# Kernel optimization log

Hardware: AMD Instinct MI355X
Metric: run time of the kernel (lower is better)

The kernel has to match this reference:

```python
import jax, jax.numpy as jnp
import numpy as np

BS, N, C = 16, 4096, 32
HID, OUT = 16, 1
N_ORBS = 64


def _linear_init(key, fan_in, fan_out):
    # torch nn.Linear default: U(-1/sqrt(fan_in), 1/sqrt(fan_in)) for W and b
    kw, kb = jax.random.split(key)
    bound = 1.0 / np.sqrt(fan_in)
    W = jax.random.uniform(kw, (fan_in, fan_out), minval=-bound, maxval=bound, dtype=jnp.float32)
    b = jax.random.uniform(kb, (fan_out,), minval=-bound, maxval=bound, dtype=jnp.float32)
    return W, b


def setup_inputs() -> dict:
    key = jax.random.key(0)
    ks = jax.random.split(key, 8)
    coords = jax.random.normal(ks[0], (BS, N, 2, 2), dtype=jnp.float32)
    # orbit identifiers live at coords[:, :, 1, 1]; draw from a fixed discrete set
    orb_ids = jax.random.randint(ks[1], (BS, N), 0, N_ORBS).astype(jnp.float32)
    # guarantee all N_ORBS values appear so unique() has exactly N_ORBS entries
    orb_ids = orb_ids.at[0, :N_ORBS].set(jnp.arange(N_ORBS, dtype=jnp.float32))
    coords = coords.at[:, :, 1, 1].set(orb_ids)
    vals = jax.random.normal(ks[2], (BS, N, C), dtype=jnp.float32)
    mask = jax.random.bernoulli(ks[3], 0.9, (BS, N))
    W1, b1 = _linear_init(ks[4], C, HID)
    W2, b2 = _linear_init(ks[5], HID, HID)
    W3, b3 = _linear_init(ks[6], HID, OUT)
    return {"coords": coords, "vals": vals, "mask": mask,
            "W1": W1, "b1": b1, "W2": W2, "b2": b2, "W3": W3, "b3": b3,
            "n_orbs": N_ORBS}


def reference(coords, vals, mask, W1, b1, W2, b2, W3, b3, n_orbs):
    orb = coords[:, :, 1, 1]                              # (bs, n)
    # torch.unique over the whole tensor -> sorted global unique orbit values
    uniq = jnp.unique(orb, size=n_orbs)                   # (n_orbs,)
    # orbit-membership mask; einsum contraction over n == masked broadcast + sum(dim=1)
    orbs_mask = (orb[:, :, None] == uniq[None, None, :]).astype(vals.dtype)  # (bs, n, n_orbs)
    masked_vals = jnp.where(mask[..., None], vals, jnp.zeros((), vals.dtype))  # (bs, n, c)
    agg_orbs = jnp.einsum('bnk,bnc->bkc', orbs_mask, masked_vals)              # (bs, n_orbs, c)
    empty_orbs = agg_orbs.sum(axis=-1) == 0               # (bs, n_orbs)
    h = jax.nn.relu(agg_orbs @ W1 + b1)
    h = jax.nn.relu(h @ W2 + b2)
    transf = h @ W3 + b3                                  # (bs, n_orbs, out_dim)
    transf = jnp.where(empty_orbs[..., None], jnp.zeros((), transf.dtype), transf)
    return transf.sum(axis=1)                             # (bs, out_dim)
```

## Files before the change

### kernel.cpp

```cpp
#include <hip/hip_runtime.h>

#define BS     16
#define NPTS   4096
#define CH     32
#define HID    16
#define NORB   64
#define SLICES 16
#define PPB    (NPTS / SLICES)

__global__ __launch_bounds__(256) void gigp_agg(
    const float* __restrict__ coords,
    const float* __restrict__ vals,
    const int*   __restrict__ mask,
    float*       __restrict__ part)
{
    __shared__ float vlds[PPB][CH];
    __shared__ int   klds[PPB];

    const int tid   = threadIdx.x;
    const int b     = blockIdx.x >> 4;
    const int slice = blockIdx.x & (SLICES - 1);
    const size_t gbase = (size_t)b * NPTS + slice * PPB;

    const float4* v4  = (const float4*)vals + gbase * (CH / 4);
    float4*       vl4 = (float4*)&vlds[0][0];
    #pragma unroll
    for (int i = 0; i < PPB * CH / (4 * 256); ++i)
        vl4[tid + i * 256] = v4[tid + i * 256];

    {
        const size_t gi = gbase + tid;
        const int k = (int)coords[gi * 4 + 3];
        klds[tid] = mask[gi] ? k : NORB;
    }
    __syncthreads();

    const int myk  = tid >> 2;
    const int c0   = (tid & 3) * 8;
    const int lane = tid & 63;
    const int wo_s = __builtin_amdgcn_readfirstlane((tid >> 6) << 4);

    float acc[8] = {0, 0, 0, 0, 0, 0, 0, 0};

    for (int base = 0; base < PPB; base += 64) {
        const int kreg = klds[base + lane];
        #pragma unroll 8
        for (int j = 0; j < 64; ++j) {
            const int kn = __builtin_amdgcn_readlane(kreg, j);
            if ((unsigned)(kn - wo_s) < 16u) {
                if (kn == myk) {
                    const float4 u0 = *(const float4*)&vlds[base + j][c0];
                    const float4 u1 = *(const float4*)&vlds[base + j][c0 + 4];
                    acc[0] += u0.x; acc[1] += u0.y; acc[2] += u0.z; acc[3] += u0.w;
                    acc[4] += u1.x; acc[5] += u1.y; acc[6] += u1.z; acc[7] += u1.w;
                }
            }
        }
    }

    float4* dst = (float4*)(part + ((size_t)b * SLICES + slice) * NORB * CH);
    const int fi = myk * 8 + (tid & 3) * 2;
    dst[fi]     = make_float4(acc[0], acc[1], acc[2], acc[3]);
    dst[fi + 1] = make_float4(acc[4], acc[5], acc[6], acc[7]);
}

__global__ __launch_bounds__(256) void gigp_mlp(
    const float* __restrict__ part,
    const float* __restrict__ W1, const float* __restrict__ b1,
    const float* __restrict__ W2, const float* __restrict__ b2,
    const float* __restrict__ W3, const float* __restrict__ b3,
    float*       __restrict__ out)
{
    __shared__ float agg[NORB][CH + 1];
    __shared__ float wbuf[832];
    const int b   = blockIdx.x;
    const int tid = threadIdx.x;

    for (int i = tid; i < 817; i += 256) {
        float w;
        if      (i < 512) w = W1[i];
        else if (i < 528) w = b1[i - 512];
        else if (i < 784) w = W2[i - 528];
        else if (i < 800) w = b2[i - 784];
        else if (i < 816) w = W3[i - 800];
        else              w = b3[0];
        wbuf[i] = w;
    }

    const float4* src = (const float4*)(part + (size_t)b * SLICES * NORB * CH);
    float4 a0 = make_float4(0.f, 0.f, 0.f, 0.f);
    float4 a1 = make_float4(0.f, 0.f, 0.f, 0.f);
    #pragma unroll
    for (int s = 0; s < SLICES; ++s) {
        const float4 t0 = src[s * (NORB * CH / 4) + tid];
        const float4 t1 = src[s * (NORB * CH / 4) + tid + 256];
        a0.x += t0.x; a0.y += t0.y; a0.z += t0.z; a0.w += t0.w;
        a1.x += t1.x; a1.y += t1.y; a1.z += t1.z; a1.w += t1.w;
    }
    {
        const int e0 = tid, e1 = tid + 256;
        const int k0 = e0 >> 3, c0 = (e0 & 7) * 4;
        const int k1 = e1 >> 3, c1 = (e1 & 7) * 4;
        agg[k0][c0 + 0] = a0.x; agg[k0][c0 + 1] = a0.y;
        agg[k0][c0 + 2] = a0.z; agg[k0][c0 + 3] = a0.w;
        agg[k1][c1 + 0] = a1.x; agg[k1][c1 + 1] = a1.y;
        agg[k1][c1 + 2] = a1.z; agg[k1][c1 + 3] = a1.w;
    }
    __syncthreads();

    if (tid < NORB) {
        const int k = tid;
        const float* Wl1 = wbuf;
        const float* bl1 = wbuf + 512;
        const float* Wl2 = wbuf + 528;
        const float* bl2 = wbuf + 784;
        const float* Wl3 = wbuf + 800;
        const float  bl3 = wbuf[816];

        float chsum = 0.0f;
        #pragma unroll
        for (int cc = 0; cc < CH; ++cc) chsum += agg[k][cc];

        float h1[HID];
        #pragma unroll
        for (int j = 0; j < HID; ++j) h1[j] = bl1[j];
        #pragma unroll
        for (int cc = 0; cc < CH; ++cc) {
            const float x = agg[k][cc];
            #pragma unroll
            for (int j = 0; j < HID; ++j)
                h1[j] += x * Wl1[cc * HID + j];
        }
        #pragma unroll
        for (int j = 0; j < HID; ++j) h1[j] = h1[j] > 0.0f ? h1[j] : 0.0f;

        float h2[HID];
        #pragma unroll
        for (int j = 0; j < HID; ++j) h2[j] = bl2[j];
        #pragma unroll
        for (int i = 0; i < HID; ++i) {
            const float x = h1[i];
            #pragma unroll
            for (int j = 0; j < HID; ++j)
                h2[j] += x * Wl2[i * HID + j];
        }
        float o = bl3;
        #pragma unroll
        for (int i = 0; i < HID; ++i) {
            const float x = h2[i] > 0.0f ? h2[i] : 0.0f;
            o += x * Wl3[i];
        }
        o = (chsum == 0.0f) ? 0.0f : o;

        #pragma unroll
        for (int off = 32; off > 0; off >>= 1)
            o += __shfl_down(o, off);
        if (k == 0) out[b] = o;
    }
}

extern "C" void kernel_launch(void* const* d_in, const int* in_sizes, int n_in,
                              void* d_out, int out_size, void* d_ws, size_t ws_size,
                              hipStream_t stream) {
    const float* coords = (const float*)d_in[0];
    const float* vals   = (const float*)d_in[1];
    const int*   mask   = (const int*)d_in[2];
    const float* W1     = (const float*)d_in[3];
    const float* b1     = (const float*)d_in[4];
    const float* W2     = (const float*)d_in[5];
    const float* b2     = (const float*)d_in[6];
    const float* W3     = (const float*)d_in[7];
    const float* b3     = (const float*)d_in[8];
    float* out  = (float*)d_out;
    float* part = (float*)d_ws;

    gigp_agg<<<BS * SLICES, 256, 0, stream>>>(coords, vals, mask, part);
    gigp_mlp<<<BS, 256, 0, stream>>>(part, W1, b1, W2, b2, W3, b3, out);
}
```

Before: 98.05 us.

## Fuse aggregation and MLP kernels via cooperative grid sync

Merges the two kernels into one cooperative launch. Every block writes its partial sums, the whole grid synchronizes, and then the first BS blocks reduce the partials and run the MLP. This removes a kernel launch and the gap between the two dependent kernels. In exchange it adds a grid-wide barrier, uses more LDS per block, and depends on all 256 blocks being co-resident.

```diff
diff --git a/kernel.cpp b/kernel.cpp
--- a/kernel.cpp
+++ b/kernel.cpp
@@ -1,4 +1,7 @@
 #include <hip/hip_runtime.h>
+#include <hip/hip_cooperative_groups.h>
+
+namespace cg = cooperative_groups;
 
 #define BS     16
 #define NPTS   4096
@@ -8,18 +11,24 @@
 #define SLICES 16
 #define PPB    (NPTS / SLICES)
 
-__global__ __launch_bounds__(256) void gigp_agg(
+__global__ __launch_bounds__(256) void gigp_fused(
     const float* __restrict__ coords,
     const float* __restrict__ vals,
     const int*   __restrict__ mask,
-    float*       __restrict__ part)
+    float*       __restrict__ part,
+    const float* __restrict__ W1, const float* __restrict__ b1,
+    const float* __restrict__ W2, const float* __restrict__ b2,
+    const float* __restrict__ W3, const float* __restrict__ b3,
+    float*       __restrict__ out)
 {
     __shared__ float vlds[PPB][CH];
     __shared__ int   klds[PPB];
-
+    __shared__ float agg[NORB][CH + 1];
+    __shared__ float wbuf[832];
     const int tid   = threadIdx.x;
-    const int b     = blockIdx.x >> 4;
-    const int slice = blockIdx.x & (SLICES - 1);
+    const int bid   = blockIdx.x;
+    const int b     = bid >> 4;
+    const int slice = bid & (SLICES - 1);
     const size_t gbase = (size_t)b * NPTS + slice * PPB;
 
     const float4* v4  = (const float4*)vals + gbase * (CH / 4);
@@ -58,36 +67,31 @@
         }
     }
 
-    float4* dst = (float4*)(part + ((size_t)b * SLICES + slice) * NORB * CH);
-    const int fi = myk * 8 + (tid & 3) * 2;
-    dst[fi]     = make_float4(acc[0], acc[1], acc[2], acc[3]);
-    dst[fi + 1] = make_float4(acc[4], acc[5], acc[6], acc[7]);
-}
-
-__global__ __launch_bounds__(256) void gigp_mlp(
-    const float* __restrict__ part,
-    const float* __restrict__ W1, const float* __restrict__ b1,
-    const float* __restrict__ W2, const float* __restrict__ b2,
-    const float* __restrict__ W3, const float* __restrict__ b3,
-    float*       __restrict__ out)
-{
-    __shared__ float agg[NORB][CH + 1];
-    __shared__ float wbuf[832];
-    const int b   = blockIdx.x;
-    const int tid = threadIdx.x;
-
-    for (int i = tid; i < 817; i += 256) {
-        float w;
-        if      (i < 512) w = W1[i];
-        else if (i < 528) w = b1[i - 512];
-        else if (i < 784) w = W2[i - 528];
-        else if (i < 800) w = b2[i - 784];
-        else if (i < 816) w = W3[i - 800];
-        else              w = b3[0];
-        wbuf[i] = w;
+    {
+        float4* dst = (float4*)(part + ((size_t)b * SLICES + slice) * NORB * CH);
+        const int fi = myk * 8 + (tid & 3) * 2;
+        dst[fi]     = make_float4(acc[0], acc[1], acc[2], acc[3]);
+        dst[fi + 1] = make_float4(acc[4], acc[5], acc[6], acc[7]);
     }
 
-    const float4* src = (const float4*)(part + (size_t)b * SLICES * NORB * CH);
+    if (bid < BS) {
+        for (int i = tid; i < 817; i += 256) {
+            float w;
+            if      (i < 512) w = W1[i];
+            else if (i < 528) w = b1[i - 512];
+            else if (i < 784) w = W2[i - 528];
+            else if (i < 800) w = b2[i - 784];
+            else if (i < 816) w = W3[i - 800];
+            else              w = b3[0];
+            wbuf[i] = w;
+        }
+    }
+
+    cg::this_grid().sync();
+
+    if (bid >= BS) return;
+
+    const float4* src = (const float4*)(part + (size_t)bid * SLICES * NORB * CH);
     float4 a0 = make_float4(0.f, 0.f, 0.f, 0.f);
     float4 a1 = make_float4(0.f, 0.f, 0.f, 0.f);
     #pragma unroll
@@ -99,12 +103,12 @@
     }
     {
         const int e0 = tid, e1 = tid + 256;
-        const int k0 = e0 >> 3, c0 = (e0 & 7) * 4;
-        const int k1 = e1 >> 3, c1 = (e1 & 7) * 4;
-        agg[k0][c0 + 0] = a0.x; agg[k0][c0 + 1] = a0.y;
-        agg[k0][c0 + 2] = a0.z; agg[k0][c0 + 3] = a0.w;
-        agg[k1][c1 + 0] = a1.x; agg[k1][c1 + 1] = a1.y;
-        agg[k1][c1 + 2] = a1.z; agg[k1][c1 + 3] = a1.w;
+        const int k0 = e0 >> 3, cc0 = (e0 & 7) * 4;
+        const int k1 = e1 >> 3, cc1 = (e1 & 7) * 4;
+        agg[k0][cc0 + 0] = a0.x; agg[k0][cc0 + 1] = a0.y;
+        agg[k0][cc0 + 2] = a0.z; agg[k0][cc0 + 3] = a0.w;
+        agg[k1][cc1 + 0] = a1.x; agg[k1][cc1 + 1] = a1.y;
+        agg[k1][cc1 + 2] = a1.z; agg[k1][cc1 + 3] = a1.w;
     }
     __syncthreads();
 
@@ -155,7 +159,7 @@
         #pragma unroll
         for (int off = 32; off > 0; off >>= 1)
             o += __shfl_down(o, off);
-        if (k == 0) out[b] = o;
+        if (k == 0) out[bid] = o;
     }
 }
 
@@ -174,6 +178,9 @@
     float* out  = (float*)d_out;
     float* part = (float*)d_ws;
 
-    gigp_agg<<<BS * SLICES, 256, 0, stream>>>(coords, vals, mask, part);
-    gigp_mlp<<<BS, 256, 0, stream>>>(part, W1, b1, W2, b2, W3, b3, out);
+    void* args[] = {(void*)&coords, (void*)&vals, (void*)&mask, (void*)&part,
+                    (void*)&W1, (void*)&b1, (void*)&W2, (void*)&b2,
+                    (void*)&W3, (void*)&b3, (void*)&out};
+    hipLaunchCooperativeKernel((const void*)gigp_fused,
+                               dim3(BS * SLICES), dim3(256), args, 0, stream);
 }
```

Measured after the change: 148.2 us. 51.2% more time.
